# Performance work log

Hardware: AMD Instinct MI355X
Metric: run time of the kernel (lower is better)

## Reference

```python
import jax, jax.numpy as jnp
import numpy as np

N_NODES = 50000
N_EDGES = 800000
N_CEDGES = 200000
D = 128


def setup_inputs() -> dict:
    key = jax.random.key(0)
    ks = jax.random.split(key, 8)
    return {
        "node_attr": jax.random.normal(ks[0], (N_NODES, D), jnp.float32),
        "edge_attr": jax.random.normal(ks[1], (N_EDGES, D), jnp.float32),
        "edge_contact_attr": jax.random.normal(ks[2], (N_CEDGES, D), jnp.float32),
        "receivers_idx": jax.random.randint(ks[3], (N_EDGES,), 0, N_NODES),
        "receivers_contact_idx": jax.random.randint(ks[4], (N_CEDGES,), 0, N_NODES),
        "W1": jax.random.normal(ks[5], (3 * D, D), jnp.float32) * (1.0 / np.sqrt(3 * D)),
        "b1": jnp.zeros((D,), jnp.float32),
        "W2": jax.random.normal(ks[6], (D, D), jnp.float32) * (1.0 / np.sqrt(D)),
        "b2": jnp.zeros((D,), jnp.float32),
        "ln_gamma": jnp.ones((D,), jnp.float32),
        "ln_beta": jnp.zeros((D,), jnp.float32),
    }


def _scatter_mean(vals, idx, num_segments):
    # scatter_mean semantics: mean over contributions; 0 for empty segments
    sums = jax.ops.segment_sum(vals, idx, num_segments=num_segments)  # [N, D]
    cnt = jax.ops.segment_sum(jnp.ones((vals.shape[0],), vals.dtype), idx,
                              num_segments=num_segments)  # [N]
    return sums / jnp.maximum(cnt, 1.0)[:, None]


def _layer_norm(x, gamma, beta, eps=1e-5):
    mu = jnp.mean(x, axis=-1, keepdims=True)
    var = jnp.var(x, axis=-1, keepdims=True)
    return (x - mu) * jax.lax.rsqrt(var + eps) * gamma + beta


def reference(node_attr, edge_attr, edge_contact_attr, receivers_idx,
              receivers_contact_idx, W1, b1, W2, b2, ln_gamma, ln_beta):
    n = node_attr.shape[0]
    agg_mesh = _scatter_mean(edge_attr, receivers_idx, n)                 # [N, D]
    agg_contact = _scatter_mean(edge_contact_attr, receivers_contact_idx, n)  # [N, D]
    concat = jnp.concatenate([node_attr, agg_mesh, agg_contact], axis=-1)  # [N, 3D]
    h = jax.nn.relu(concat @ W1 + b1)
    h = h @ W2 + b2
    new_node_attr = _layer_norm(h, ln_gamma, ln_beta)
    return new_node_attr
```

## Files before the change

kernel.cpp:

```cpp
#include <hip/hip_runtime.h>

#define N_NODES 50000
#define N_EDGES 800000
#define N_CEDGES 200000
#define D 128
#define CAP_M 64
#define CAP_C 32

typedef short s16x4 __attribute__((ext_vector_type(4)));
typedef short s16x8 __attribute__((ext_vector_type(8)));
typedef float f32x4 __attribute__((ext_vector_type(4)));
typedef __bf16 bf16x8 __attribute__((ext_vector_type(8)));
typedef int i32x4 __attribute__((ext_vector_type(4)));

__device__ __forceinline__ unsigned short f2bf(float f) {
    unsigned int u = __builtin_bit_cast(unsigned int, f);
    u = u + 0x7fffu + ((u >> 16) & 1u);
    return (unsigned short)(u >> 16);
}

__device__ __forceinline__ f32x4 ntload(const float* p) {
    return __builtin_nontemporal_load((const f32x4*)p);
}

__global__ void fill_pack_kernel(const int* __restrict__ rm, const int* __restrict__ rc,
                                 int* __restrict__ cnt_m, int* __restrict__ cnt_c,
                                 int* __restrict__ csr_m, int* __restrict__ csr_c,
                                 const float* __restrict__ W1, const float* __restrict__ W2,
                                 s16x8* __restrict__ wp1, s16x8* __restrict__ wp2) {
    if (blockIdx.x < 977) {
        int t = blockIdx.x * blockDim.x + threadIdx.x;
        if (t < N_EDGES / 4) {
            i32x4 r = *(const i32x4*)(rm + t * 4);
#pragma unroll
            for (int j = 0; j < 4; ++j) {
                int pos = atomicAdd(&cnt_m[r[j]], 1);
                if (pos < CAP_M) csr_m[r[j] * CAP_M + pos] = t * 4 + j;
            }
        } else if (t < N_EDGES / 4 + N_CEDGES / 4) {
            int t2 = t - N_EDGES / 4;
            i32x4 r = *(const i32x4*)(rc + t2 * 4);
#pragma unroll
            for (int j = 0; j < 4; ++j) {
                int pos = atomicAdd(&cnt_c[r[j]], 1);
                if (pos < CAP_C) csr_c[r[j] * CAP_C + pos] = t2 * 4 + j;
            }
        }
    } else {
        int t = (blockIdx.x - 977) * blockDim.x + threadIdx.x;
        if (t < 12 * 8 * 64) {
            int ks = t >> 9, rem = t & 511, nt = rem >> 6, l = rem & 63;
            int kb = ks * 32 + ((l >> 4) * 8), col = nt * 16 + (l & 15);
            s16x8 v;
#pragma unroll
            for (int j = 0; j < 8; ++j) v[j] = (short)f2bf(W1[(size_t)(kb + j) * D + col]);
            wp1[t] = v;
        } else if (t < (12 + 4) * 8 * 64) {
            int t2 = t - 12 * 8 * 64;
            int ks = t2 >> 9, rem = t2 & 511, nt = rem >> 6, l = rem & 63;
            int kb = ks * 32 + ((l >> 4) * 8), col = nt * 16 + (l & 15);
            s16x8 v;
#pragma unroll
            for (int j = 0; j < 8; ++j) v[j] = (short)f2bf(W2[(size_t)(kb + j) * D + col]);
            wp2[t2] = v;
        }
    }
}

__launch_bounds__(256)
__global__ void gather_kernel(const float* __restrict__ edge_attr,
                              const float* __restrict__ cedge_attr,
                              const int* __restrict__ csr_m, const int* __restrict__ csr_c,
                              const int* __restrict__ cnt_m, const int* __restrict__ cnt_c,
                              unsigned short* __restrict__ aggm, unsigned short* __restrict__ aggc) {
    const int lane = threadIdx.x & 63;
    const int n = blockIdx.x * 4 + (threadIdx.x >> 6);
    if (n >= N_NODES) return;
    const int h = lane >> 5;
    const int sub = lane & 31;
    const int c0 = sub * 4;

    const int cntm = cnt_m[n];
    const int cntc = cnt_c[n];
    const int cm = cntm < CAP_M ? cntm : CAP_M;
    const int cc = cntc < CAP_C ? cntc : CAP_C;
    int sm = lane < cm ? lane : (cm > 0 ? cm - 1 : 0);
    int sc = lane < cc ? lane : (cc > 0 ? cc - 1 : 0);
    const int idxm = csr_m[n * CAP_M + sm];
    const int idxc = csr_c[n * CAP_C + sc];

    {
        f32x4 A0 = (f32x4)0.f, A1 = (f32x4)0.f, A2 = (f32x4)0.f, A3 = (f32x4)0.f;
        int i = 0;
        for (; i + 8 <= cm; i += 8) {
            int e0 = __shfl(idxm, i + h);
            int e1 = __shfl(idxm, i + 2 + h);
            int e2 = __shfl(idxm, i + 4 + h);
            int e3 = __shfl(idxm, i + 6 + h);
            A0 += ntload(edge_attr + (size_t)e0 * D + c0);
            A1 += ntload(edge_attr + (size_t)e1 * D + c0);
            A2 += ntload(edge_attr + (size_t)e2 * D + c0);
            A3 += ntload(edge_attr + (size_t)e3 * D + c0);
        }
        if (i + 4 <= cm) {
            int e0 = __shfl(idxm, i + h);
            int e1 = __shfl(idxm, i + 2 + h);
            A0 += ntload(edge_attr + (size_t)e0 * D + c0);
            A1 += ntload(edge_attr + (size_t)e1 * D + c0);
            i += 4;
        }
        if (i + 2 <= cm) {
            int e0 = __shfl(idxm, i + h);
            A2 += ntload(edge_attr + (size_t)e0 * D + c0);
            i += 2;
        }
        if (i < cm) {
            int e0 = __shfl(idxm, i);
            if (h == 0) A3 += ntload(edge_attr + (size_t)e0 * D + c0);
        }
        f32x4 A = (A0 + A1) + (A2 + A3);
#pragma unroll
        for (int k = 0; k < 4; ++k) A[k] += __shfl_xor(A[k], 32);
        const float inv = 1.0f / fmaxf((float)cntm, 1.0f);
        if (lane < 32) {
            s16x4 pv;
#pragma unroll
            for (int k = 0; k < 4; ++k) pv[k] = (short)f2bf(A[k] * inv);
            *(s16x4*)(aggm + (size_t)n * D + c0) = pv;
        }
    }
    {
        f32x4 A0 = (f32x4)0.f, A1 = (f32x4)0.f, A2 = (f32x4)0.f, A3 = (f32x4)0.f;
        int i = 0;
        for (; i + 8 <= cc; i += 8) {
            int e0 = __shfl(idxc, i + h);
            int e1 = __shfl(idxc, i + 2 + h);
            int e2 = __shfl(idxc, i + 4 + h);
            int e3 = __shfl(idxc, i + 6 + h);
            A0 += ntload(cedge_attr + (size_t)e0 * D + c0);
            A1 += ntload(cedge_attr + (size_t)e1 * D + c0);
            A2 += ntload(cedge_attr + (size_t)e2 * D + c0);
            A3 += ntload(cedge_attr + (size_t)e3 * D + c0);
        }
        if (i + 4 <= cc) {
            int e0 = __shfl(idxc, i + h);
            int e1 = __shfl(idxc, i + 2 + h);
            A0 += ntload(cedge_attr + (size_t)e0 * D + c0);
            A1 += ntload(cedge_attr + (size_t)e1 * D + c0);
            i += 4;
        }
        if (i + 2 <= cc) {
            int e0 = __shfl(idxc, i + h);
            A2 += ntload(cedge_attr + (size_t)e0 * D + c0);
            i += 2;
        }
        if (i < cc) {
            int e0 = __shfl(idxc, i);
            if (h == 0) A3 += ntload(cedge_attr + (size_t)e0 * D + c0);
        }
        f32x4 A = (A0 + A1) + (A2 + A3);
#pragma unroll
        for (int k = 0; k < 4; ++k) A[k] += __shfl_xor(A[k], 32);
        const float inv = 1.0f / fmaxf((float)cntc, 1.0f);
        if (lane < 32) {
            s16x4 pv;
#pragma unroll
            for (int k = 0; k < 4; ++k) pv[k] = (short)f2bf(A[k] * inv);
            *(s16x4*)(aggc + (size_t)n * D + c0) = pv;
        }
    }
}

__launch_bounds__(256, 3)
__global__ void gemm_fused_kernel(const float* __restrict__ node_attr,
                                  const unsigned short* __restrict__ aggm,
                                  const unsigned short* __restrict__ aggc,
                                  const s16x8* __restrict__ wp1,
                                  const s16x8* __restrict__ wp2,
                                  const float* __restrict__ b1,
                                  const float* __restrict__ b2,
                                  const float* __restrict__ gamma,
                                  const float* __restrict__ beta,
                                  float* __restrict__ out) {
    __shared__ short Xl[64 * 392];
    short* Hl = Xl;
    const int tid = threadIdx.x;
    const int lane = tid & 63;
    const int w = tid >> 6;
    const int m0 = blockIdx.x * 64;

#pragma unroll
    for (int it = 0; it < 8; ++it) {
        int c = tid + it * 256;
        int row = c >> 5, c4 = c & 31;
        float4 v = make_float4(0.f, 0.f, 0.f, 0.f);
        if (m0 + row < N_NODES) v = *(const float4*)(node_attr + (size_t)(m0 + row) * D + c4 * 4);
        s16x4 sv;
        sv[0] = (short)f2bf(v.x); sv[1] = (short)f2bf(v.y);
        sv[2] = (short)f2bf(v.z); sv[3] = (short)f2bf(v.w);
        *(s16x4*)&Xl[row * 392 + c4 * 4] = sv;
    }
#pragma unroll
    for (int it = 0; it < 4; ++it) {
        int c = tid + it * 256;
        int row = c >> 4, c8 = c & 15;
        s16x8 vm = (s16x8)0, vc = (s16x8)0;
        if (m0 + row < N_NODES) {
            vm = *(const s16x8*)(aggm + (size_t)(m0 + row) * D + c8 * 8);
            vc = *(const s16x8*)(aggc + (size_t)(m0 + row) * D + c8 * 8);
        }
        *(s16x8*)&Xl[row * 392 + 128 + c8 * 8] = vm;
        *(s16x8*)&Xl[row * 392 + 256 + c8 * 8] = vc;
    }
    __syncthreads();

    const int rrow = w * 16 + (lane & 15);
    const int kg = (lane >> 4) * 8;

    f32x4 acc[8];
#pragma unroll
    for (int nt = 0; nt < 8; ++nt) acc[nt] = (f32x4)0.0f;
#pragma unroll
    for (int ks = 0; ks < 12; ++ks) {
        s16x8 a = *(const s16x8*)&Xl[rrow * 392 + ks * 32 + kg];
#pragma unroll
        for (int nt = 0; nt < 8; ++nt) {
            s16x8 b = wp1[(ks * 8 + nt) * 64 + lane];
            acc[nt] = __builtin_amdgcn_mfma_f32_16x16x32_bf16(
                __builtin_bit_cast(bf16x8, a), __builtin_bit_cast(bf16x8, b), acc[nt], 0, 0, 0);
        }
    }
    __syncthreads();

#pragma unroll
    for (int nt = 0; nt < 8; ++nt) {
        float bias = b1[nt * 16 + (lane & 15)];
#pragma unroll
        for (int j = 0; j < 4; ++j) {
            float v = fmaxf(acc[nt][j] + bias, 0.0f);
            int r = w * 16 + (lane >> 4) * 4 + j;
            Hl[r * 136 + nt * 16 + (lane & 15)] = (short)f2bf(v);
        }
    }
    f32x4 acc2[8];
#pragma unroll
    for (int nt = 0; nt < 8; ++nt) acc2[nt] = (f32x4)0.0f;
#pragma unroll
    for (int ks = 0; ks < 4; ++ks) {
        s16x8 a = *(const s16x8*)&Hl[rrow * 136 + ks * 32 + kg];
#pragma unroll
        for (int nt = 0; nt < 8; ++nt) {
            s16x8 b = wp2[(ks * 8 + nt) * 64 + lane];
            acc2[nt] = __builtin_amdgcn_mfma_f32_16x16x32_bf16(
                __builtin_bit_cast(bf16x8, a), __builtin_bit_cast(bf16x8, b), acc2[nt], 0, 0, 0);
        }
    }
    float g8[8], be8[8], b28[8];
#pragma unroll
    for (int nt = 0; nt < 8; ++nt) {
        int c = nt * 16 + (lane & 15);
        g8[nt] = gamma[c]; be8[nt] = beta[c]; b28[nt] = b2[c];
    }
#pragma unroll
    for (int j = 0; j < 4; ++j) {
        float vv[8];
        float s = 0.f, qq = 0.f;
#pragma unroll
        for (int nt = 0; nt < 8; ++nt) {
            float v = acc2[nt][j] + b28[nt];
            vv[nt] = v; s += v; qq += v * v;
        }
#pragma unroll
        for (int m = 1; m < 16; m <<= 1) {
            s += __shfl_xor(s, m);
            qq += __shfl_xor(qq, m);
        }
        float mu = s * (1.0f / D);
        float var = qq * (1.0f / D) - mu * mu;
        float rs = rsqrtf(var + 1e-5f);
        int r = m0 + w * 16 + (lane >> 4) * 4 + j;
        if (r < N_NODES) {
#pragma unroll
            for (int nt = 0; nt < 8; ++nt)
                out[(size_t)r * D + nt * 16 + (lane & 15)] = (vv[nt] - mu) * rs * g8[nt] + be8[nt];
        }
    }
}


extern "C" void kernel_launch(void* const* d_in, const int* in_sizes, int n_in,
                              void* d_out, int out_size, void* d_ws, size_t ws_size,
                              hipStream_t stream) {
    const float* node_attr  = (const float*)d_in[0];
    const float* edge_attr  = (const float*)d_in[1];
    const float* cedge_attr = (const float*)d_in[2];
    const int*   rm         = (const int*)d_in[3];
    const int*   rc         = (const int*)d_in[4];
    const float* W1         = (const float*)d_in[5];
    const float* b1         = (const float*)d_in[6];
    const float* W2         = (const float*)d_in[7];
    const float* b2         = (const float*)d_in[8];
    const float* gamma      = (const float*)d_in[9];
    const float* beta       = (const float*)d_in[10];
    float* out = (float*)d_out;

    char* ws = (char*)d_ws;
    int* cnt_m  = (int*)(ws + 0);
    int* cnt_c  = (int*)(ws + 200704);
    int* csr_m  = (int*)(ws + 401408);
    int* csr_c  = (int*)(ws + 13201408);
    s16x8* wp1  = (s16x8*)(ws + 19601408);
    s16x8* wp2  = (s16x8*)(ws + 19699712);
    unsigned short* aggm = (unsigned short*)(ws + 19732480);
    unsigned short* aggc = (unsigned short*)(ws + 32532480);

    hipMemsetAsync(ws, 0, 401408, stream);

    fill_pack_kernel<<<1009, 256, 0, stream>>>(rm, rc, cnt_m, cnt_c, csr_m, csr_c,
                                               W1, W2, wp1, wp2);
    gather_kernel<<<12500, 256, 0, stream>>>(edge_attr, cedge_attr, csr_m, csr_c,
                                             cnt_m, cnt_c, aggm, aggc);
    gemm_fused_kernel<<<782, 256, 0, stream>>>(node_attr, aggm, aggc,
                                               wp1, wp2, b1, b2, gamma, beta, out);
}
```

Before: 213.5 us.

## Map one node per half-wavefront in gather and issue mesh and contact loads together

The gather kernel now assigns each 32-lane half-wave its own node, so a 64-lane wave handles two nodes and the grid is halved. This removes the cross-half shuffle reduction. Mesh edges up to 24 and contact edges up to 8 are loaded in one fully unrolled predicated burst, so both streams have many loads in flight at once. Higher-degree tails fall back to wave-uniform loops guarded by __any. The cost is more accumulator registers and predicated-off shuffles for low-degree nodes, and two nodes in one wave with unequal degrees can diverge.

```diff
diff --git a/kernel.cpp b/kernel.cpp
--- a/kernel.cpp
+++ b/kernel.cpp
@@ -73,101 +73,74 @@
                               const int* __restrict__ csr_m, const int* __restrict__ csr_c,
                               const int* __restrict__ cnt_m, const int* __restrict__ cnt_c,
                               unsigned short* __restrict__ aggm, unsigned short* __restrict__ aggc) {
-    const int lane = threadIdx.x & 63;
-    const int n = blockIdx.x * 4 + (threadIdx.x >> 6);
-    if (n >= N_NODES) return;
+    const int tid = threadIdx.x;
+    const int lane = tid & 63;
     const int h = lane >> 5;
     const int sub = lane & 31;
     const int c0 = sub * 4;
-
+    const int hb = h << 5;
+    const int n = blockIdx.x * 8 + (tid >> 6) * 2 + h;
+
+    const int idxm = csr_m[n * CAP_M + sub];
+    const int idxc = csr_c[n * CAP_C + sub];
     const int cntm = cnt_m[n];
     const int cntc = cnt_c[n];
     const int cm = cntm < CAP_M ? cntm : CAP_M;
     const int cc = cntc < CAP_C ? cntc : CAP_C;
-    int sm = lane < cm ? lane : (cm > 0 ? cm - 1 : 0);
-    int sc = lane < cc ? lane : (cc > 0 ? cc - 1 : 0);
-    const int idxm = csr_m[n * CAP_M + sm];
-    const int idxc = csr_c[n * CAP_C + sc];
+
+    f32x4 A0 = (f32x4)0.f, A1 = (f32x4)0.f, A2 = (f32x4)0.f, A3 = (f32x4)0.f;
+    f32x4 A4 = (f32x4)0.f, A5 = (f32x4)0.f, A6 = (f32x4)0.f, A7 = (f32x4)0.f;
+    f32x4 C0 = (f32x4)0.f, C1 = (f32x4)0.f, C2 = (f32x4)0.f, C3 = (f32x4)0.f;
+    f32x4* Am[8] = {&A0, &A1, &A2, &A3, &A4, &A5, &A6, &A7};
+    f32x4* Cm[4] = {&C0, &C1, &C2, &C3};
+
+#pragma unroll
+    for (int r = 0; r < 24; ++r) {
+        int e = __shfl(idxm, hb + r);
+        if (r < cm) *Am[r & 7] += ntload(edge_attr + (size_t)e * D + c0);
+    }
+#pragma unroll
+    for (int r = 0; r < 8; ++r) {
+        int e = __shfl(idxc, hb + r);
+        if (r < cc) *Cm[r & 3] += ntload(cedge_attr + (size_t)e * D + c0);
+    }
+
+    if (__any(cm > 24)) {
+#pragma unroll
+        for (int r = 24; r < 32; ++r) {
+            int e = __shfl(idxm, hb + r);
+            if (r < cm) A0 += ntload(edge_attr + (size_t)e * D + c0);
+        }
+        if (__any(cm > 32)) {
+            int idxm2 = csr_m[n * CAP_M + 32 + sub];
+            for (int r = 32; r < CAP_M && __any(r < cm); ++r) {
+                int e = __shfl(idxm2, hb + (r - 32));
+                if (r < cm) A1 += ntload(edge_attr + (size_t)e * D + c0);
+            }
+        }
+    }
+    if (__any(cc > 8)) {
+        for (int r = 8; r < CAP_C && __any(r < cc); ++r) {
+            int e = __shfl(idxc, hb + r);
+            if (r < cc) C0 += ntload(cedge_attr + (size_t)e * D + c0);
+        }
+    }
 
     {
-        f32x4 A0 = (f32x4)0.f, A1 = (f32x4)0.f, A2 = (f32x4)0.f, A3 = (f32x4)0.f;
-        int i = 0;
-        for (; i + 8 <= cm; i += 8) {
-            int e0 = __shfl(idxm, i + h);
-            int e1 = __shfl(idxm, i + 2 + h);
-            int e2 = __shfl(idxm, i + 4 + h);
-            int e3 = __shfl(idxm, i + 6 + h);
-            A0 += ntload(edge_attr + (size_t)e0 * D + c0);
-            A1 += ntload(edge_attr + (size_t)e1 * D + c0);
-            A2 += ntload(edge_attr + (size_t)e2 * D + c0);
-            A3 += ntload(edge_attr + (size_t)e3 * D + c0);
-        }
-        if (i + 4 <= cm) {
-            int e0 = __shfl(idxm, i + h);
-            int e1 = __shfl(idxm, i + 2 + h);
-            A0 += ntload(edge_attr + (size_t)e0 * D + c0);
-            A1 += ntload(edge_attr + (size_t)e1 * D + c0);
-            i += 4;
-        }
-        if (i + 2 <= cm) {
-            int e0 = __shfl(idxm, i + h);
-            A2 += ntload(edge_attr + (size_t)e0 * D + c0);
-            i += 2;
-        }
-        if (i < cm) {
-            int e0 = __shfl(idxm, i);
-            if (h == 0) A3 += ntload(edge_attr + (size_t)e0 * D + c0);
-        }
-        f32x4 A = (A0 + A1) + (A2 + A3);
-#pragma unroll
-        for (int k = 0; k < 4; ++k) A[k] += __shfl_xor(A[k], 32);
+        f32x4 A = ((A0 + A1) + (A2 + A3)) + ((A4 + A5) + (A6 + A7));
         const float inv = 1.0f / fmaxf((float)cntm, 1.0f);
-        if (lane < 32) {
-            s16x4 pv;
-#pragma unroll
-            for (int k = 0; k < 4; ++k) pv[k] = (short)f2bf(A[k] * inv);
-            *(s16x4*)(aggm + (size_t)n * D + c0) = pv;
-        }
+        s16x4 pv;
+#pragma unroll
+        for (int k = 0; k < 4; ++k) pv[k] = (short)f2bf(A[k] * inv);
+        *(s16x4*)(aggm + (size_t)n * D + c0) = pv;
     }
     {
-        f32x4 A0 = (f32x4)0.f, A1 = (f32x4)0.f, A2 = (f32x4)0.f, A3 = (f32x4)0.f;
-        int i = 0;
-        for (; i + 8 <= cc; i += 8) {
-            int e0 = __shfl(idxc, i + h);
-            int e1 = __shfl(idxc, i + 2 + h);
-            int e2 = __shfl(idxc, i + 4 + h);
-            int e3 = __shfl(idxc, i + 6 + h);
-            A0 += ntload(cedge_attr + (size_t)e0 * D + c0);
-            A1 += ntload(cedge_attr + (size_t)e1 * D + c0);
-            A2 += ntload(cedge_attr + (size_t)e2 * D + c0);
-            A3 += ntload(cedge_attr + (size_t)e3 * D + c0);
-        }
-        if (i + 4 <= cc) {
-            int e0 = __shfl(idxc, i + h);
-            int e1 = __shfl(idxc, i + 2 + h);
-            A0 += ntload(cedge_attr + (size_t)e0 * D + c0);
-            A1 += ntload(cedge_attr + (size_t)e1 * D + c0);
-            i += 4;
-        }
-        if (i + 2 <= cc) {
-            int e0 = __shfl(idxc, i + h);
-            A2 += ntload(cedge_attr + (size_t)e0 * D + c0);
-            i += 2;
-        }
-        if (i < cc) {
-            int e0 = __shfl(idxc, i);
-            if (h == 0) A3 += ntload(cedge_attr + (size_t)e0 * D + c0);
-        }
-        f32x4 A = (A0 + A1) + (A2 + A3);
-#pragma unroll
-        for (int k = 0; k < 4; ++k) A[k] += __shfl_xor(A[k], 32);
+        f32x4 C = (C0 + C1) + (C2 + C3);
         const float inv = 1.0f / fmaxf((float)cntc, 1.0f);
-        if (lane < 32) {
-            s16x4 pv;
-#pragma unroll
-            for (int k = 0; k < 4; ++k) pv[k] = (short)f2bf(A[k] * inv);
-            *(s16x4*)(aggc + (size_t)n * D + c0) = pv;
-        }
+        s16x4 pv;
+#pragma unroll
+        for (int k = 0; k < 4; ++k) pv[k] = (short)f2bf(C[k] * inv);
+        *(s16x4*)(aggc + (size_t)n * D + c0) = pv;
     }
 }
 
@@ -318,8 +291,8 @@
 
     fill_pack_kernel<<<1009, 256, 0, stream>>>(rm, rc, cnt_m, cnt_c, csr_m, csr_c,
                                                W1, W2, wp1, wp2);
-    gather_kernel<<<12500, 256, 0, stream>>>(edge_attr, cedge_attr, csr_m, csr_c,
-                                             cnt_m, cnt_c, aggm, aggc);
+    gather_kernel<<<6250, 256, 0, stream>>>(edge_attr, cedge_attr, csr_m, csr_c,
+                                            cnt_m, cnt_c, aggm, aggc);
     gemm_fused_kernel<<<782, 256, 0, stream>>>(node_attr, aggm, aggc,
                                                wp1, wp2, b1, b2, gamma, beta, out);
 }
```

After: 221.8 us. 1.04x slower.
